# Performance work log

Hardware: AMD Instinct MI355X
Metric: run time of the kernel (lower is better)

## Reference

```python
import jax, jax.numpy as jnp
import numpy as np

COMMITMENT_COST = 0.25
DECAY = 0.99
EPSILON = 1e-05
NUM_EMBEDDINGS = 1024
EMBEDDING_DIM = 256


def setup_inputs() -> dict:
    key = jax.random.key(0)
    k1, k2, k3 = jax.random.split(key, 3)
    inputs = jax.random.normal(k1, (64, 32, 32, EMBEDDING_DIM), dtype=jnp.float32)
    embedding = jax.random.normal(k2, (NUM_EMBEDDINGS, EMBEDDING_DIM), dtype=jnp.float32)
    ema_cluster_size = jnp.zeros((NUM_EMBEDDINGS,), dtype=jnp.float32)
    ema_w = jax.random.normal(k3, (NUM_EMBEDDINGS, EMBEDDING_DIM), dtype=jnp.float32)
    return {"inputs": inputs, "embedding": embedding,
            "ema_cluster_size": ema_cluster_size, "ema_w": ema_w}


def reference(inputs, embedding, ema_cluster_size, ema_w):
    K, D = embedding.shape
    orig_shape = inputs.shape
    flat = inputs.reshape(-1, D)  # [N, D]

    distances = (jnp.sum(flat * flat, axis=-1, keepdims=True)
                 + jnp.sum(embedding * embedding, axis=-1)[None, :]
                 - 2.0 * flat @ embedding.T)
    idx = jnp.argmin(distances, axis=-1)  # [N] int

    # one-hot @ embedding == gather
    quantized = embedding[idx].reshape(orig_shape)

    # EMA state update (training mode)
    counts = jax.ops.segment_sum(jnp.ones_like(idx, dtype=flat.dtype), idx,
                                 num_segments=K)  # encodings.sum(0)
    new_cluster_size = DECAY * ema_cluster_size + (1.0 - DECAY) * counts
    dw = jax.ops.segment_sum(flat, idx, num_segments=K)  # encodings.T @ flat
    new_ema_w = DECAY * ema_w + (1.0 - DECAY) * dw
    n = jnp.sum(new_cluster_size)
    normalized = (new_cluster_size + EPSILON) / (n + K * EPSILON) * n
    new_embedding = new_ema_w / normalized[:, None]

    commitment_loss = COMMITMENT_COST * jnp.mean((quantized - inputs) ** 2)
    codebook_loss = jnp.mean((quantized - inputs) ** 2)

    # straight-through estimator
    quantized_st = inputs + jax.lax.stop_gradient(quantized - inputs)
    codes = idx.reshape(orig_shape[:-1])
    return (quantized_st, codes, commitment_loss, codebook_loss,
            new_embedding, new_cluster_size, new_ema_w)
```

## Files before the change

kernel.cpp:

```cpp
#include <hip/hip_runtime.h>

#define NV 65536
#define KN 1024
#define DD 256
#define DECAY_F 0.99f
#define OMD_F (1.0f - 0.99f)
#define EPS_F 1e-5f

typedef __attribute__((ext_vector_type(8))) short short8;
typedef __attribute__((ext_vector_type(16))) float f32x16;

__device__ __forceinline__ void gl_lds16(const void* g, void* l) {
  __builtin_amdgcn_global_load_lds(
      (const __attribute__((address_space(1))) unsigned int*)g,
      (__attribute__((address_space(3))) unsigned int*)l, 16, 0, 0);
}

__device__ __forceinline__ void bf16_split(float v, short& hi, short& lo) {
  unsigned u = __float_as_uint(v);
  unsigned hr = (u + 0x7FFFu + ((u >> 16) & 1u)) >> 16;
  float hf = __uint_as_float(hr << 16);
  float rem = v - hf;
  unsigned u2 = __float_as_uint(rem);
  unsigned lr = (u2 + 0x7FFFu + ((u2 >> 16) & 1u)) >> 16;
  hi = (short)hr;
  lo = (short)lr;
}

__device__ __forceinline__ void split8(float4 a, float4 b, short8& h,
                                       short8& l) {
  float v[8] = {a.x, a.y, a.z, a.w, b.x, b.y, b.z, b.w};
  #pragma unroll
  for (int j = 0; j < 8; j++) {
    short hh, ll;
    bf16_split(v[j], hh, ll);
    h[j] = hh; l[j] = ll;
  }
}

__global__ __launch_bounds__(256) void prep_small(
    const float* __restrict__ emb, short* __restrict__ eT,
    float* __restrict__ eSq, float* __restrict__ zeroBase) {
  const int b = blockIdx.x;
  if (b < 32) {
    const int cc = b >> 3, dc = b & 7;
    const int c = threadIdx.x;
    const float* src = emb + (cc * 256 + c) * 256 + dc * 32;
    short* tile = eT + b * 16384;
    #pragma unroll
    for (int db = 0; db < 4; db++) {
      float v[8];
      *(float4*)(v + 0) = *(const float4*)(src + db * 8);
      *(float4*)(v + 4) = *(const float4*)(src + db * 8 + 4);
      short8 h, l;
      #pragma unroll
      for (int j = 0; j < 8; j++) {
        short hh, ll;
        bf16_split(v[j], hh, ll);
        h[j] = hh; l[j] = ll;
      }
      *(short8*)(tile + ((0 * 4 + db) * 256 + c) * 8) = h;
      *(short8*)(tile + ((1 * 4 + db) * 256 + c) * 8) = l;
    }
  } else if (b < 288) {
    const int lane = threadIdx.x & 63;
    const int row = (b - 32) * 4 + (threadIdx.x >> 6);
    const float4 v = *(const float4*)(emb + row * DD + lane * 4);
    float s = v.x * v.x + v.y * v.y + v.z * v.z + v.w * v.w;
    #pragma unroll
    for (int off = 32; off > 0; off >>= 1) s += __shfl_down(s, off, 64);
    if (lane == 0) eSq[row] = s;
  } else {
    const int i = ((b - 288) * 256 + threadIdx.x) * 4;
    if (i < 262400)
      *(float4*)(zeroBase + i) = make_float4(0.0f, 0.0f, 0.0f, 0.0f);
  }
}

__global__ __launch_bounds__(256, 2) void argmin_mfma(
    const float* __restrict__ x, const float* __restrict__ emb,
    const short* __restrict__ eT, const float* __restrict__ eSq,
    float* __restrict__ outQ, float* __restrict__ outCodes,
    int* __restrict__ idxFinal, float* __restrict__ sseSlots) {
  __shared__ __align__(16) char uS[67584];
  __shared__ float eSqS[1024];
  __shared__ float sseW[4];

  float2* dbAll = (float2*)uS;

  const int tid = threadIdx.x;
  const int lane = tid & 63;
  const int wid = tid >> 6;
  const int l31 = lane & 31;
  const int lh = lane >> 5;
  const int qBase = blockIdx.x * 128 + wid * 32;

  *(float4*)(eSqS + tid * 4) = *(const float4*)(eSq + tid * 4);
  __syncthreads();

  float2* dbW = dbAll + wid * (64 * 33);

  float b1d = 3.4e38f, b2d = 3.4e38f;
  int b1k = 0, b2k = 1;

  const int qRow = (qBase + l31) * DD;

  const int wbase = wid * 1024;
  const int lane16 = lane * 16;

  for (int cc = 0; cc < 4; cc++) {
    __syncthreads();

    {
      const char* src = (const char*)(eT + (cc * 8 + 0) * 16384);
      #pragma unroll
      for (int i = 0; i < 8; i++)
        gl_lds16(src + i * 4096 + wbase + lane16, uS + i * 4096 + wbase);
    }

    f32x16 acc[8];
    #pragma unroll
    for (int ct = 0; ct < 8; ct++)
      #pragma unroll
      for (int i = 0; i < 16; i++) acc[ct][i] = 0.0f;

    float es2[8];
    #pragma unroll
    for (int ct = 0; ct < 8; ct++) es2[ct] = eSqS[cc * 256 + ct * 32 + l31];

    for (int dc = 0; dc < 8; dc++) {
      const int cur = dc & 1;
      const short* eS = (const short*)(uS + cur * 32768);

      float4 ra0, rb0, ra1, rb1;
      {
        const float* xr = x + qRow + dc * 32 + lh * 8;
        ra0 = *(const float4*)(xr);
        rb0 = *(const float4*)(xr + 4);
        ra1 = *(const float4*)(xr + 16);
        rb1 = *(const float4*)(xr + 20);
      }
      __builtin_amdgcn_sched_barrier(0);

      if (dc < 7) {
        const char* src = (const char*)(eT + (cc * 8 + dc + 1) * 16384);
        char* dst = uS + (cur ^ 1) * 32768;
        #pragma unroll
        for (int i = 0; i < 8; i++)
          gl_lds16(src + i * 4096 + wbase + lane16, dst + i * 4096 + wbase);
        asm volatile("s_waitcnt vmcnt(12)" ::: "memory");
      } else {
        asm volatile("s_waitcnt vmcnt(4)" ::: "memory");
      }
      __builtin_amdgcn_s_barrier();
      asm volatile("" ::: "memory");

      short8 ahi0, alo0, ahi1, alo1;
      split8(ra0, rb0, ahi0, alo0);
      split8(ra1, rb1, ahi1, alo1);

      #pragma unroll
      for (int ks = 0; ks < 2; ks++) {
        const short8 ahi = ks ? ahi1 : ahi0;
        const short8 alo = ks ? alo1 : alo0;
        const int db = ks * 2 + lh;
        #pragma unroll
        for (int ct = 0; ct < 8; ct++) {
          const int cL = ct * 32 + l31;
          const short8 bhi = *(const short8*)(eS + ((0 * 4 + db) * 256 + cL) * 8);
          const short8 blo = *(const short8*)(eS + ((1 * 4 + db) * 256 + cL) * 8);
          acc[ct] = __builtin_amdgcn_mfma_f32_32x32x16_bf16(ahi, bhi, acc[ct], 0, 0, 0);
          acc[ct] = __builtin_amdgcn_mfma_f32_32x32x16_bf16(ahi, blo, acc[ct], 0, 0, 0);
          acc[ct] = __builtin_amdgcn_mfma_f32_32x32x16_bf16(alo, bhi, acc[ct], 0, 0, 0);
        }
      }

      asm volatile("" ::: "memory");
      __builtin_amdgcn_s_barrier();
      asm volatile("" ::: "memory");
    }

    __syncthreads();

    #pragma unroll
    for (int r = 0; r < 16; r++) {
      const int row = (r & 3) + 8 * (r >> 2) + 4 * lh;
      float cb1 = 3.4e38f, cb2 = 3.4e38f;
      int ck1 = 0, ck2 = 0;
      #pragma unroll
      for (int ct = 0; ct < 8; ct++) {
        const float dd = es2[ct] - 2.0f * acc[ct][r];
        const int k = cc * 256 + ct * 32 + l31;
        if (dd < cb1) { cb2 = cb1; ck2 = ck1; cb1 = dd; ck1 = k; }
        else if (dd < cb2) { cb2 = dd; ck2 = k; }
      }
      dbW[(l31 * 2 + 0) * 33 + row] = make_float2(cb1, __int_as_float(ck1));
      dbW[(l31 * 2 + 1) * 33 + row] = make_float2(cb2, __int_as_float(ck2));
    }
    __syncthreads();

    #pragma unroll
    for (int i = 0; i < 32; i++) {
      const float2 c = dbW[(lh * 32 + i) * 33 + l31];
      const float dd = c.x;
      const int k = __float_as_int(c.y);
      if (dd < b1d) { b2d = b1d; b2k = b1k; b1d = dd; b1k = k; }
      else if (dd < b2d) { b2d = dd; b2k = k; }
    }
  }

  {
    const float p1d = __shfl_xor(b1d, 32, 64);
    const int p1k = __shfl_xor(b1k, 32, 64);
    const float p2d = __shfl_xor(b2d, 32, 64);
    const int p2k = __shfl_xor(b2k, 32, 64);
    if ((p1d < b1d) || (p1d == b1d && p1k < b1k)) {
      b2d = b1d; b2k = b1k; b1d = p1d; b1k = p1k;
    } else if ((p1d < b2d) || (p1d == b2d && p1k < b2k)) {
      b2d = p1d; b2k = p1k;
    }
    if ((p2d < b1d) || (p2d == b1d && p2k < b1k)) {
      b2d = b1d; b2k = b1k; b1d = p2d; b1k = p2k;
    } else if ((p2d < b2d) || (p2d == b2d && p2k < b2k)) {
      b2d = p2d; b2k = p2k;
    }
  }

  float sseAcc = 0.0f;
  for (int qb = 0; qb < 32; qb += 4) {
    int k1[4], k2[4];
    #pragma unroll
    for (int j = 0; j < 4; j++) {
      k1[j] = __shfl(b1k, qb + j, 64);
      k2[j] = __shfl(b2k, qb + j, 64);
    }
    float4 xv[4], e1[4], e2[4];
    #pragma unroll
    for (int j = 0; j < 4; j++) {
      const int n = qBase + qb + j;
      xv[j] = *(const float4*)(x + n * DD + lane * 4);
      e1[j] = *(const float4*)(emb + k1[j] * DD + lane * 4);
      e2[j] = *(const float4*)(emb + k2[j] * DD + lane * 4);
    }
    #pragma unroll
    for (int j = 0; j < 4; j++) {
      const int n = qBase + qb + j;
      float p1 = e1[j].x * (e1[j].x - 2.0f * xv[j].x) +
                 e1[j].y * (e1[j].y - 2.0f * xv[j].y) +
                 e1[j].z * (e1[j].z - 2.0f * xv[j].z) +
                 e1[j].w * (e1[j].w - 2.0f * xv[j].w);
      float p2 = e2[j].x * (e2[j].x - 2.0f * xv[j].x) +
                 e2[j].y * (e2[j].y - 2.0f * xv[j].y) +
                 e2[j].z * (e2[j].z - 2.0f * xv[j].z) +
                 e2[j].w * (e2[j].w - 2.0f * xv[j].w);
      #pragma unroll
      for (int m = 32; m > 0; m >>= 1) {
        p1 += __shfl_xor(p1, m, 64);
        p2 += __shfl_xor(p2, m, 64);
      }
      const bool pick2 = (p2 < p1) || (p2 == p1 && k2[j] < k1[j]);
      const int ksel = pick2 ? k2[j] : k1[j];
      const float4 ev = pick2 ? e2[j] : e1[j];

      *(float4*)(outQ + n * DD + lane * 4) = ev;

      const float d0 = ev.x - xv[j].x, d1 = ev.y - xv[j].y,
                  d2 = ev.z - xv[j].z, d3 = ev.w - xv[j].w;
      float s = d0 * d0 + d1 * d1 + d2 * d2 + d3 * d3;
      #pragma unroll
      for (int m = 32; m > 0; m >>= 1) s += __shfl_down(s, m, 64);
      if (lane == 0) {
        sseAcc += s;
        idxFinal[n] = ksel;
        outCodes[n] = (float)ksel;
      }
    }
  }
  if (lane == 0) sseW[wid] = sseAcc;
  __syncthreads();
  if (tid == 0) {
    const float t = (sseW[0] + sseW[1]) + (sseW[2] + sseW[3]);
    atomicAdd(&sseSlots[blockIdx.x & 255], t);
  }
}

__global__ __launch_bounds__(1024) void scan_scatter_fin(
    const int* __restrict__ idxFinal, const float* __restrict__ ema_cs,
    const float* __restrict__ sseSlots, int* __restrict__ perm,
    float* __restrict__ norm, float* __restrict__ outCS,
    float* __restrict__ outLoss) {
  __shared__ int hist[1024];
  __shared__ int si[1024];
  __shared__ int cur[1024];
  __shared__ float red[1024];
  const int t = threadIdx.x;

  hist[t] = 0;
  __syncthreads();
  for (int i = t; i < NV; i += 1024) atomicAdd(&hist[idxFinal[i]], 1);
  __syncthreads();
  const int v = hist[t];

  si[t] = v;
  __syncthreads();
  #pragma unroll
  for (int off = 1; off < 1024; off <<= 1) {
    const int add = (t >= off) ? si[t - off] : 0;
    __syncthreads();
    si[t] += add;
    __syncthreads();
  }
  cur[t] = si[t] - v;

  const float ncs = DECAY_F * ema_cs[t] + OMD_F * (float)v;
  outCS[t] = ncs;
  red[t] = ncs;
  __syncthreads();
  #pragma unroll
  for (int s = 512; s > 0; s >>= 1) {
    if (t < s) red[t] += red[t + s];
    __syncthreads();
  }
  const float n = red[0];
  __syncthreads();
  norm[t] = (ncs + EPS_F) / (n + (float)KN * EPS_F) * n;

  red[t] = (t < 256) ? sseSlots[t] : 0.0f;
  __syncthreads();
  #pragma unroll
  for (int s = 512; s > 0; s >>= 1) {
    if (t < s) red[t] += red[t + s];
    __syncthreads();
  }
  if (t == 0) {
    const float mse = red[0] * (1.0f / 16777216.0f);
    outLoss[0] = 0.25f * mse;
    outLoss[1] = mse;
  }
  __syncthreads();

  for (int i = t; i < NV; i += 1024) {
    const int k = idxFinal[i];
    const int pos = atomicAdd(&cur[k], 1);
    perm[pos] = (k << 16) | i;
  }
}

__global__ __launch_bounds__(256) void dw_sum(const float* __restrict__ x,
                                              const int* __restrict__ perm,
                                              float* __restrict__ dw) {
  __shared__ int sp[128];
  const int tid = threadIdx.x;
  if (tid < 128) sp[tid] = perm[blockIdx.x * 128 + tid];
  __syncthreads();
  const int w = tid >> 6;
  const int l = tid & 63;
  const int* wp = sp + w * 32;

  float4 acc = make_float4(0.0f, 0.0f, 0.0f, 0.0f);
  int kcur = wp[0] >> 16;

  #pragma unroll
  for (int c = 0; c < 4; c++) {
    float4 v[8];
    int kk[8];
    #pragma unroll
    for (int j = 0; j < 8; j++) {
      const int p = wp[c * 8 + j];
      kk[j] = p >> 16;
      v[j] = *(const float4*)(x + (long)(p & 0xFFFF) * DD + l * 4);
    }
    #pragma unroll
    for (int j = 0; j < 8; j++) {
      if (kk[j] != kcur) {
        float* drow = dw + kcur * DD + l * 4;
        atomicAdd(drow + 0, acc.x);
        atomicAdd(drow + 1, acc.y);
        atomicAdd(drow + 2, acc.z);
        atomicAdd(drow + 3, acc.w);
        acc = make_float4(0.0f, 0.0f, 0.0f, 0.0f);
        kcur = kk[j];
      }
      acc.x += v[j].x; acc.y += v[j].y;
      acc.z += v[j].z; acc.w += v[j].w;
    }
  }
  {
    float* drow = dw + kcur * DD + l * 4;
    atomicAdd(drow + 0, acc.x);
    atomicAdd(drow + 1, acc.y);
    atomicAdd(drow + 2, acc.z);
    atomicAdd(drow + 3, acc.w);
  }
}

__global__ __launch_bounds__(256) void finalize2(
    const float* __restrict__ ema_w, const float* __restrict__ dw,
    const float* __restrict__ norm, float* __restrict__ outEmb,
    float* __restrict__ outW) {
  const int i = blockIdx.x * 256 + threadIdx.x;
  const float nw = DECAY_F * ema_w[i] + OMD_F * dw[i];
  outW[i] = nw;
  outEmb[i] = nw / norm[i >> 8];
}

extern "C" void kernel_launch(void* const* d_in, const int* in_sizes, int n_in,
                              void* d_out, int out_size, void* d_ws, size_t ws_size,
                              hipStream_t stream) {
  const float* x = (const float*)d_in[0];
  const float* emb = (const float*)d_in[1];
  const float* ema_cs = (const float*)d_in[2];
  const float* ema_w = (const float*)d_in[3];
  float* out = (float*)d_out;
  float* ws = (float*)d_ws;

  float* eSq = ws + 0;
  float* sseSlots = ws + 1024;
  float* dw = ws + 1280;
  float* norm = ws + 263424;
  int* idxFinal = (int*)(ws + 264448);
  int* perm = (int*)(ws + 329984);

  float* outQ = out;
  float* outCodes = out + 16777216;
  float* outLoss = out + 16842752;
  float* outEmb = out + 16842754;
  float* outCS = out + 17104898;
  float* outW = out + 17105922;

  short* eT = (short*)(out + 16842756);

  prep_small<<<545, 256, 0, stream>>>(emb, eT, eSq, ws + 1024);
  argmin_mfma<<<NV / 128, 256, 0, stream>>>(x, emb, eT, eSq, outQ, outCodes,
                                            idxFinal, sseSlots);
  scan_scatter_fin<<<1, 1024, 0, stream>>>(idxFinal, ema_cs, sseSlots, perm,
                                           norm, outCS, outLoss);
  dw_sum<<<NV / 128, 256, 0, stream>>>(x, perm, dw);
  finalize2<<<KN * DD / 256, 256, 0, stream>>>(ema_w, dw, norm, outEmb, outW);
}
```

Baseline: 323.8 us.

## Fuse histogram into argmin, parallelize scatter, accumulate dw directly into ema_w output

Per-block histograms are built in the argmin kernel and merged with global atomics. The last block to finish, detected through a done counter, computes the prefix scan, the new cluster sizes, the normalisation and the loss. The single-block scan/scatter kernel is replaced by a multi-block scatter that uses global cursors. ema_w is pre-scaled by decay in the prep kernel so dw_sum can atomically add scaled sums straight into outW, which removes the dw buffer and simplifies the finalize step. The catch is a last-block tail inside argmin and extra atomics in exchange for removing a serial 1-block kernel.

```diff
diff --git a/kernel.cpp b/kernel.cpp
--- a/kernel.cpp
+++ b/kernel.cpp
@@ -39,8 +39,10 @@
 }
 
 __global__ __launch_bounds__(256) void prep_small(
-    const float* __restrict__ emb, short* __restrict__ eT,
-    float* __restrict__ eSq, float* __restrict__ zeroBase) {
+    const float* __restrict__ emb, const float* __restrict__ ema_w,
+    short* __restrict__ eT, float* __restrict__ eSq,
+    float* __restrict__ outW, float* __restrict__ sseSlots,
+    int* __restrict__ cntI, int* __restrict__ doneCnt) {
   const int b = blockIdx.x;
   if (b < 32) {
     const int cc = b >> 3, dc = b & 7;
@@ -70,21 +72,35 @@
     #pragma unroll
     for (int off = 32; off > 0; off >>= 1) s += __shfl_down(s, off, 64);
     if (lane == 0) eSq[row] = s;
+  } else if (b < 800) {
+    const int i = (b - 288) * 512 + threadIdx.x * 2;
+    const float2 w = *(const float2*)(ema_w + i);
+    float2 o;
+    o.x = DECAY_F * w.x;
+    o.y = DECAY_F * w.y;
+    *(float2*)(outW + i) = o;
   } else {
-    const int i = ((b - 288) * 256 + threadIdx.x) * 4;
-    if (i < 262400)
-      *(float4*)(zeroBase + i) = make_float4(0.0f, 0.0f, 0.0f, 0.0f);
+    const int t = threadIdx.x;
+    if (t < 256) sseSlots[t] = 0.0f;
+    #pragma unroll
+    for (int j = 0; j < 4; j++) cntI[t * 4 + j] = 0;
+    if (t == 0) *doneCnt = 0;
   }
 }
 
 __global__ __launch_bounds__(256, 2) void argmin_mfma(
     const float* __restrict__ x, const float* __restrict__ emb,
     const short* __restrict__ eT, const float* __restrict__ eSq,
-    float* __restrict__ outQ, float* __restrict__ outCodes,
-    int* __restrict__ idxFinal, float* __restrict__ sseSlots) {
+    const float* __restrict__ ema_cs, float* __restrict__ outQ,
+    float* __restrict__ outCodes, int* __restrict__ idxFinal,
+    float* __restrict__ sseSlots, int* __restrict__ cntI,
+    int* __restrict__ doneCnt, int* __restrict__ starts,
+    int* __restrict__ gcursor, float* __restrict__ norm,
+    float* __restrict__ outCS, float* __restrict__ outLoss) {
   __shared__ __align__(16) char uS[67584];
   __shared__ float eSqS[1024];
   __shared__ float sseW[4];
+  __shared__ int isLast;
 
   float2* dbAll = (float2*)uS;
 
@@ -226,6 +242,11 @@
     }
   }
 
+  __syncthreads();
+  int* lhist = (int*)uS;
+  for (int i = tid; i < 1024; i += 256) lhist[i] = 0;
+  __syncthreads();
+
   float sseAcc = 0.0f;
   for (int qb = 0; qb < 32; qb += 4) {
     int k1[4], k2[4];
@@ -273,82 +294,116 @@
         sseAcc += s;
         idxFinal[n] = ksel;
         outCodes[n] = (float)ksel;
+        atomicAdd(&lhist[ksel], 1);
       }
     }
   }
   if (lane == 0) sseW[wid] = sseAcc;
   __syncthreads();
+
+  for (int k = tid; k < 1024; k += 256) {
+    const int c = lhist[k];
+    if (c) atomicAdd(&cntI[k], c);
+  }
   if (tid == 0) {
     const float t = (sseW[0] + sseW[1]) + (sseW[2] + sseW[3]);
     atomicAdd(&sseSlots[blockIdx.x & 255], t);
   }
-}
-
-__global__ __launch_bounds__(1024) void scan_scatter_fin(
-    const int* __restrict__ idxFinal, const float* __restrict__ ema_cs,
-    const float* __restrict__ sseSlots, int* __restrict__ perm,
-    float* __restrict__ norm, float* __restrict__ outCS,
-    float* __restrict__ outLoss) {
-  __shared__ int hist[1024];
-  __shared__ int si[1024];
-  __shared__ int cur[1024];
-  __shared__ float red[1024];
-  const int t = threadIdx.x;
-
-  hist[t] = 0;
-  __syncthreads();
-  for (int i = t; i < NV; i += 1024) atomicAdd(&hist[idxFinal[i]], 1);
-  __syncthreads();
-  const int v = hist[t];
-
-  si[t] = v;
-  __syncthreads();
-  #pragma unroll
-  for (int off = 1; off < 1024; off <<= 1) {
-    const int add = (t >= off) ? si[t - off] : 0;
-    __syncthreads();
-    si[t] += add;
-    __syncthreads();
-  }
-  cur[t] = si[t] - v;
-
-  const float ncs = DECAY_F * ema_cs[t] + OMD_F * (float)v;
-  outCS[t] = ncs;
-  red[t] = ncs;
-  __syncthreads();
-  #pragma unroll
-  for (int s = 512; s > 0; s >>= 1) {
-    if (t < s) red[t] += red[t + s];
-    __syncthreads();
-  }
-  const float n = red[0];
-  __syncthreads();
-  norm[t] = (ncs + EPS_F) / (n + (float)KN * EPS_F) * n;
-
-  red[t] = (t < 256) ? sseSlots[t] : 0.0f;
-  __syncthreads();
-  #pragma unroll
-  for (int s = 512; s > 0; s >>= 1) {
-    if (t < s) red[t] += red[t + s];
+
+  __threadfence();
+  if (tid == 0) isLast = (atomicAdd(doneCnt, 1) == (int)gridDim.x - 1);
+  __syncthreads();
+  if (!isLast) return;
+  __threadfence();
+
+  int* sInt = (int*)uS;
+  float* sF = (float*)(uS + 4096);
+  const int t = tid;
+  const int4 c4 = *(const int4*)(cntI + t * 4);
+  const int l0 = c4.x, l01 = c4.x + c4.y, l012 = l01 + c4.z;
+  const int ltot = l012 + c4.w;
+  sInt[t] = ltot;
+  __syncthreads();
+  #pragma unroll
+  for (int off = 1; off < 256; off <<= 1) {
+    const int add = (t >= off) ? sInt[t - off] : 0;
+    __syncthreads();
+    sInt[t] += add;
+    __syncthreads();
+  }
+  const int excl = sInt[t] - ltot;
+  starts[t * 4 + 0] = excl;          gcursor[t * 4 + 0] = excl;
+  starts[t * 4 + 1] = excl + l0;     gcursor[t * 4 + 1] = excl + l0;
+  starts[t * 4 + 2] = excl + l01;    gcursor[t * 4 + 2] = excl + l01;
+  starts[t * 4 + 3] = excl + l012;   gcursor[t * 4 + 3] = excl + l012;
+
+  const float4 ecs = *(const float4*)(ema_cs + t * 4);
+  float nc[4];
+  nc[0] = DECAY_F * ecs.x + OMD_F * (float)c4.x;
+  nc[1] = DECAY_F * ecs.y + OMD_F * (float)c4.y;
+  nc[2] = DECAY_F * ecs.z + OMD_F * (float)c4.z;
+  nc[3] = DECAY_F * ecs.w + OMD_F * (float)c4.w;
+  *(float4*)(outCS + t * 4) = make_float4(nc[0], nc[1], nc[2], nc[3]);
+  sF[t] = nc[0] + nc[1] + nc[2] + nc[3];
+  __syncthreads();
+  #pragma unroll
+  for (int s = 128; s > 0; s >>= 1) {
+    if (t < s) sF[t] += sF[t + s];
+    __syncthreads();
+  }
+  const float nTot = sF[0];
+  __syncthreads();
+  const float den = nTot + (float)KN * EPS_F;
+  float4 nm;
+  nm.x = (nc[0] + EPS_F) / den * nTot;
+  nm.y = (nc[1] + EPS_F) / den * nTot;
+  nm.z = (nc[2] + EPS_F) / den * nTot;
+  nm.w = (nc[3] + EPS_F) / den * nTot;
+  *(float4*)(norm + t * 4) = nm;
+
+  sF[t] = sseSlots[t];
+  __syncthreads();
+  #pragma unroll
+  for (int s = 128; s > 0; s >>= 1) {
+    if (t < s) sF[t] += sF[t + s];
     __syncthreads();
   }
   if (t == 0) {
-    const float mse = red[0] * (1.0f / 16777216.0f);
+    const float mse = sF[0] * (1.0f / 16777216.0f);
     outLoss[0] = 0.25f * mse;
     outLoss[1] = mse;
   }
-  __syncthreads();
-
-  for (int i = t; i < NV; i += 1024) {
-    const int k = idxFinal[i];
-    const int pos = atomicAdd(&cur[k], 1);
-    perm[pos] = (k << 16) | i;
-  }
+}
+
+__global__ __launch_bounds__(256) void scatter_kernel(
+    const int* __restrict__ idxFinal, int* __restrict__ gcursor,
+    int* __restrict__ perm) {
+  __shared__ int lh[1024];
+  __shared__ int gbase[1024];
+  const int t = threadIdx.x;
+  #pragma unroll
+  for (int j = 0; j < 4; j++) lh[t * 4 + j] = 0;
+  __syncthreads();
+
+  const int n = blockIdx.x * 256 + t;
+  const int k = idxFinal[n];
+  const int r = atomicAdd(&lh[k], 1);
+  __syncthreads();
+
+  #pragma unroll
+  for (int j = 0; j < 4; j++) {
+    const int kk = t * 4 + j;
+    const int c = lh[kk];
+    if (c) gbase[kk] = atomicAdd(&gcursor[kk], c);
+  }
+  __syncthreads();
+
+  perm[gbase[k] + r] = (k << 16) | n;
 }
 
 __global__ __launch_bounds__(256) void dw_sum(const float* __restrict__ x,
                                               const int* __restrict__ perm,
-                                              float* __restrict__ dw) {
+                                              float* __restrict__ outW) {
   __shared__ int sp[128];
   const int tid = threadIdx.x;
   if (tid < 128) sp[tid] = perm[blockIdx.x * 128 + tid];
@@ -373,11 +428,11 @@
     #pragma unroll
     for (int j = 0; j < 8; j++) {
       if (kk[j] != kcur) {
-        float* drow = dw + kcur * DD + l * 4;
-        atomicAdd(drow + 0, acc.x);
-        atomicAdd(drow + 1, acc.y);
-        atomicAdd(drow + 2, acc.z);
-        atomicAdd(drow + 3, acc.w);
+        float* drow = outW + kcur * DD + l * 4;
+        atomicAdd(drow + 0, OMD_F * acc.x);
+        atomicAdd(drow + 1, OMD_F * acc.y);
+        atomicAdd(drow + 2, OMD_F * acc.z);
+        atomicAdd(drow + 3, OMD_F * acc.w);
         acc = make_float4(0.0f, 0.0f, 0.0f, 0.0f);
         kcur = kk[j];
       }
@@ -386,22 +441,19 @@
     }
   }
   {
-    float* drow = dw + kcur * DD + l * 4;
-    atomicAdd(drow + 0, acc.x);
-    atomicAdd(drow + 1, acc.y);
-    atomicAdd(drow + 2, acc.z);
-    atomicAdd(drow + 3, acc.w);
-  }
-}
-
-__global__ __launch_bounds__(256) void finalize2(
-    const float* __restrict__ ema_w, const float* __restrict__ dw,
-    const float* __restrict__ norm, float* __restrict__ outEmb,
-    float* __restrict__ outW) {
+    float* drow = outW + kcur * DD + l * 4;
+    atomicAdd(drow + 0, OMD_F * acc.x);
+    atomicAdd(drow + 1, OMD_F * acc.y);
+    atomicAdd(drow + 2, OMD_F * acc.z);
+    atomicAdd(drow + 3, OMD_F * acc.w);
+  }
+}
+
+__global__ __launch_bounds__(256) void emb_div(
+    const float* __restrict__ outW, const float* __restrict__ norm,
+    float* __restrict__ outEmb) {
   const int i = blockIdx.x * 256 + threadIdx.x;
-  const float nw = DECAY_F * ema_w[i] + OMD_F * dw[i];
-  outW[i] = nw;
-  outEmb[i] = nw / norm[i >> 8];
+  outEmb[i] = outW[i] / norm[i >> 8];
 }
 
 extern "C" void kernel_launch(void* const* d_in, const int* in_sizes, int n_in,
@@ -416,10 +468,13 @@
 
   float* eSq = ws + 0;
   float* sseSlots = ws + 1024;
-  float* dw = ws + 1280;
-  float* norm = ws + 263424;
-  int* idxFinal = (int*)(ws + 264448);
-  int* perm = (int*)(ws + 329984);
+  int* cntI = (int*)(ws + 1280);
+  int* doneCnt = (int*)(ws + 2304);
+  float* norm = ws + 2432;
+  int* starts = (int*)(ws + 3456);
+  int* gcursor = (int*)(ws + 4480);
+  int* idxFinal = (int*)(ws + 5504);
+  int* perm = (int*)(ws + 71040);
 
   float* outQ = out;
   float* outCodes = out + 16777216;
@@ -430,11 +485,12 @@
 
   short* eT = (short*)(out + 16842756);
 
-  prep_small<<<545, 256, 0, stream>>>(emb, eT, eSq, ws + 1024);
-  argmin_mfma<<<NV / 128, 256, 0, stream>>>(x, emb, eT, eSq, outQ, outCodes,
-                                            idxFinal, sseSlots);
-  scan_scatter_fin<<<1, 1024, 0, stream>>>(idxFinal, ema_cs, sseSlots, perm,
-                                           norm, outCS, outLoss);
-  dw_sum<<<NV / 128, 256, 0, stream>>>(x, perm, dw);
-  finalize2<<<KN * DD / 256, 256, 0, stream>>>(ema_w, dw, norm, outEmb, outW);
-}
+  prep_small<<<801, 256, 0, stream>>>(emb, ema_w, eT, eSq, outW, sseSlots,
+                                      cntI, doneCnt);
+  argmin_mfma<<<NV / 128, 256, 0, stream>>>(
+      x, emb, eT, eSq, ema_cs, outQ, outCodes, idxFinal, sseSlots, cntI,
+      doneCnt, starts, gcursor, norm, outCS, outLoss);
+  scatter_kernel<<<NV / 256, 256, 0, stream>>>(idxFinal, gcursor, perm);
+  dw_sum<<<NV / 128, 256, 0, stream>>>(x, perm, outW);
+  emb_div<<<KN * DD / 256, 256, 0, stream>>>(outW, norm, outEmb);
+}
```

After: 362.8 us. +12.0%, slower.
